# Performance work log

Hardware: AMD Instinct MI355X
Metric: run time of the kernel (lower is better)

## Reference

```python
import jax, jax.numpy as jnp
import numpy as np

N = 131072          # total nodes
E = 4194304         # edges (avg degree 32)
SUB = 16            # size_subgraph_samples
HID = 256


def _gcn_norm(src, dst, n):
    # add self-loops
    loops = jnp.arange(n, dtype=src.dtype)
    src = jnp.concatenate([src, loops])
    dst = jnp.concatenate([dst, loops])
    deg = jax.ops.segment_sum(jnp.ones_like(dst, dtype=jnp.float32), dst, num_segments=n)
    dinv = jnp.where(deg > 0, jax.lax.rsqrt(deg), 0.0)
    norm = dinv[src] * dinv[dst]  # [E+N]
    return src, dst, norm


def _gcn_conv(x, W, b, src, dst, norm, n):
    h = x @ W                                  # [N, out]
    msg = h[src] * norm[:, None]               # gather + scale
    agg = jax.ops.segment_sum(msg, dst, num_segments=n)
    return agg + b


def setup_inputs() -> dict:
    key = jax.random.key(0)
    ks = jax.random.split(key, 6)
    x = jax.random.normal(ks[0], (N, 128), dtype=jnp.float32)
    edge_index = jax.random.randint(ks[1], (2, E), 0, N, dtype=jnp.int64)
    W1 = jax.random.normal(ks[2], (128, HID), dtype=jnp.float32) * (1.0 / np.sqrt(128))
    b1 = jnp.zeros((HID,), dtype=jnp.float32)
    W2 = jax.random.normal(ks[3], (HID, HID), dtype=jnp.float32) * (1.0 / np.sqrt(HID))
    b2 = jnp.zeros((HID,), dtype=jnp.float32)
    Wout = jax.random.normal(ks[4], (HID * SUB, 1), dtype=jnp.float32) * (1.0 / np.sqrt(HID * SUB))
    bout = jnp.zeros((1,), dtype=jnp.float32)
    return {"x": x, "edge_index": edge_index, "W1": W1, "b1": b1,
            "W2": W2, "b2": b2, "Wout": Wout, "bout": bout}


def reference(x, edge_index, W1, b1, W2, b2, Wout, bout):
    n = x.shape[0]
    src, dst, norm = _gcn_norm(edge_index[0], edge_index[1], n)
    h = jax.nn.relu(_gcn_conv(x, W1, b1, src, dst, norm, n))
    h = jax.nn.relu(_gcn_conv(h, W2, b2, src, dst, norm, n))
    h = h.reshape(n // SUB, SUB * h.shape[1])   # [8192, 4096]
    return h @ Wout + bout                       # [8192, 1]
```

## Files before the change

### kernel.cpp

```cpp
#include <hip/hip_runtime.h>
#include <stdint.h>

#define NN 131072
#define NE 4194304
#define BKT 256
#define BKT_SH 9
#define BCAP 20480

typedef __bf16 bf16x8 __attribute__((ext_vector_type(8)));
typedef float  floatx4 __attribute__((ext_vector_type(4)));
typedef unsigned short u16x8 __attribute__((ext_vector_type(8)));

__device__ __forceinline__ float bf2f(unsigned short u) {
  union { unsigned int i; float f; } v; v.i = ((unsigned int)u) << 16; return v.f;
}
__device__ __forceinline__ unsigned short f2bf(float f) {
  union { float f; unsigned int i; } v; v.f = f;
  unsigned int r = v.i + 0x7fffu + ((v.i >> 16) & 1u);
  return (unsigned short)(r >> 16);
}


__global__ __launch_bounds__(256) void k_bzero(int* __restrict__ bktCnt) {
  bktCnt[threadIdx.x] = 0;
}

__global__ __launch_bounds__(1024) void k_bucket(const int* __restrict__ src,
                                                 const int* __restrict__ dst,
                                                 int* __restrict__ bktCnt,
                                                 unsigned int* __restrict__ bktBuf) {
  __shared__ int hist[BKT];
  __shared__ int base[BKT];
  const int t = threadIdx.x;
  if (t < BKT) hist[t] = 0;
  __syncthreads();
  const int e0 = (blockIdx.x * 1024 + t);
  const int4 s = ((const int4*)src)[e0];
  const int4 d = ((const int4*)dst)[e0];
  const int b0 = ((unsigned)d.x) >> BKT_SH, b1 = ((unsigned)d.y) >> BKT_SH;
  const int b2 = ((unsigned)d.z) >> BKT_SH, b3 = ((unsigned)d.w) >> BKT_SH;
  const int r0 = atomicAdd(&hist[b0], 1);
  const int r1 = atomicAdd(&hist[b1], 1);
  const int r2 = atomicAdd(&hist[b2], 1);
  const int r3 = atomicAdd(&hist[b3], 1);
  __syncthreads();
  if (t < BKT) base[t] = atomicAdd(&bktCnt[t], hist[t]);
  __syncthreads();
  const unsigned p0 = (((unsigned)s.x) << BKT_SH) | (d.x & 511);
  const unsigned p1 = (((unsigned)s.y) << BKT_SH) | (d.y & 511);
  const unsigned p2 = (((unsigned)s.z) << BKT_SH) | (d.z & 511);
  const unsigned p3 = (((unsigned)s.w) << BKT_SH) | (d.w & 511);
  bktBuf[(size_t)b0 * BCAP + base[b0] + r0] = p0;
  bktBuf[(size_t)b1 * BCAP + base[b1] + r1] = p1;
  bktBuf[(size_t)b2 * BCAP + base[b2] + r2] = p2;
  bktBuf[(size_t)b3 * BCAP + base[b3] + r3] = p3;
}

__global__ __launch_bounds__(1024) void k_csr(const int* __restrict__ bktCnt,
                                              const unsigned int* __restrict__ bktBuf,
                                              int* __restrict__ row_ptr,
                                              float* __restrict__ dinv,
                                              int* __restrict__ csr) {
  __shared__ int bsum[BKT];
  __shared__ int hist[512];
  __shared__ int sc[512];
  __shared__ int cur[512];
  const int b = blockIdx.x;
  const int t = threadIdx.x;
  if (t < BKT) bsum[t] = bktCnt[t];
  if (t < 512) hist[t] = 0;
  __syncthreads();
  for (int off = 1; off < BKT; off <<= 1) {
    int v = 0;
    if (t < BKT && t >= off) v = bsum[t - off];
    __syncthreads();
    if (t < BKT) bsum[t] += v;
    __syncthreads();
  }
  const int sz = bktCnt[b];
  const int csrBase = bsum[b] - sz;
  const unsigned int* eb = bktBuf + (size_t)b * BCAP;
  for (int i = t; i < sz; i += 1024) atomicAdd(&hist[eb[i] & 511], 1);
  __syncthreads();
  if (t < 512) sc[t] = hist[t];
  __syncthreads();
  for (int off = 1; off < 512; off <<= 1) {
    int v = 0;
    if (t < 512 && t >= off) v = sc[t - off];
    __syncthreads();
    if (t < 512) sc[t] += v;
    __syncthreads();
  }
  if (t < 512) {
    const int ex = csrBase + sc[t] - hist[t];
    row_ptr[b * 512 + t] = ex;
    cur[t] = ex;
    dinv[b * 512 + t] = rsqrtf((float)(hist[t] + 1));
  }
  if (b == BKT - 1 && t == 0) row_ptr[NN] = NE;
  __syncthreads();
  for (int i = t; i < sz; i += 1024) {
    const unsigned e = eb[i];
    csr[atomicAdd(&cur[e & 511], 1)] = (int)(e >> BKT_SH);
  }
}

__global__ __launch_bounds__(256) void k_cvt(const float* __restrict__ X,
                                             unsigned short* __restrict__ Xb) {
  const int t = blockIdx.x * 256 + threadIdx.x;
  const float4 v = ((const float4*)X)[t];
  ushort4 o;
  o.x = f2bf(v.x); o.y = f2bf(v.y); o.z = f2bf(v.z); o.w = f2bf(v.w);
  ((ushort4*)Xb)[t] = o;
}

__global__ __launch_bounds__(256) void k_swizzle(const float* __restrict__ W,
                                                 unsigned short* __restrict__ Wsw) {
  const int t = blockIdx.x * 256 + threadIdx.x;
  const int k = t >> 8, n = t & 255;
  const int s = ((k >> 5) * 16 + (n >> 4)) * 512 + ((k >> 3) & 3) * 128 + (n & 15) * 8 + (k & 7);
  Wsw[s] = f2bf(W[t]);
}

__global__ __launch_bounds__(256) void agg_128(const unsigned short* __restrict__ X,
                                               const int* __restrict__ row_ptr,
                                               const int* __restrict__ csr,
                                               const float* __restrict__ dinv,
                                               unsigned short* __restrict__ Y,
                                               int node_base) {
  const int lane = threadIdx.x & 63;
  const int node = node_base + ((blockIdx.x * blockDim.x + threadIdx.x) >> 6);
  const int sub = lane >> 4;
  const int fl = lane & 15;
  const int start = row_ptr[node];
  const int end = row_ptr[node + 1];
  const float di = dinv[node];
  float a[8] = {0.f, 0.f, 0.f, 0.f, 0.f, 0.f, 0.f, 0.f};
  const unsigned short* Xf = X + fl * 8;

  for (int e = start; e < end; e += 64) {
    const int nload = min(end - e, 64);
    int s_l = node;
    float w_l = 0.0f;
    if (lane < nload) {
      s_l = __builtin_nontemporal_load(&csr[e + lane]);
      w_l = dinv[s_l];
    }
    for (int j = 0; j < nload; j += 16) {
      const int i0 = j + sub, i1 = j + 4 + sub, i2 = j + 8 + sub, i3 = j + 12 + sub;
      const int s0 = __shfl(s_l, i0); const float w0 = __shfl(w_l, i0);
      const int s1 = __shfl(s_l, i1); const float w1 = __shfl(w_l, i1);
      const int s2 = __shfl(s_l, i2); const float w2 = __shfl(w_l, i2);
      const int s3 = __shfl(s_l, i3); const float w3 = __shfl(w_l, i3);
      const u16x8 r0 = *(const u16x8*)(Xf + (size_t)s0 * 128);
      const u16x8 r1 = *(const u16x8*)(Xf + (size_t)s1 * 128);
      const u16x8 r2 = *(const u16x8*)(Xf + (size_t)s2 * 128);
      const u16x8 r3 = *(const u16x8*)(Xf + (size_t)s3 * 128);
#pragma unroll
      for (int i = 0; i < 8; ++i) a[i] = fmaf(w0, bf2f(r0[i]), a[i]);
#pragma unroll
      for (int i = 0; i < 8; ++i) a[i] = fmaf(w1, bf2f(r1[i]), a[i]);
#pragma unroll
      for (int i = 0; i < 8; ++i) a[i] = fmaf(w2, bf2f(r2[i]), a[i]);
#pragma unroll
      for (int i = 0; i < 8; ++i) a[i] = fmaf(w3, bf2f(r3[i]), a[i]);
    }
  }
#pragma unroll
  for (int i = 0; i < 8; ++i) a[i] += __shfl_xor(a[i], 16);
#pragma unroll
  for (int i = 0; i < 8; ++i) a[i] += __shfl_xor(a[i], 32);
  const u16x8 sv = *(const u16x8*)(Xf + (size_t)node * 128);
#pragma unroll
  for (int i = 0; i < 8; ++i) a[i] = fmaf(di, bf2f(sv[i]), a[i]);
  if (sub == 0) {
    u16x8 o;
#pragma unroll
    for (int i = 0; i < 8; ++i) o[i] = f2bf(di * a[i]);
    *(u16x8*)(Y + (size_t)node * 128 + fl * 8) = o;
  }
}

__global__ __launch_bounds__(256) void agg_256(const unsigned short* __restrict__ X,
                                               const int* __restrict__ row_ptr,
                                               const int* __restrict__ csr,
                                               const float* __restrict__ dinv,
                                               unsigned short* __restrict__ Y,
                                               int node_base) {
  const int lane = threadIdx.x & 63;
  const int node = node_base + ((blockIdx.x * blockDim.x + threadIdx.x) >> 6);
  const int sub = lane >> 5;
  const int fl = lane & 31;
  const int start = row_ptr[node];
  const int end = row_ptr[node + 1];
  const float di = dinv[node];
  float a[8] = {0.f, 0.f, 0.f, 0.f, 0.f, 0.f, 0.f, 0.f};
  const unsigned short* Xf = X + fl * 8;

  for (int e = start; e < end; e += 64) {
    const int nload = min(end - e, 64);
    int s_l = node;
    float w_l = 0.0f;
    if (lane < nload) {
      s_l = __builtin_nontemporal_load(&csr[e + lane]);
      w_l = dinv[s_l];
    }
    for (int j = 0; j < nload; j += 8) {
      const int i0 = j + sub, i1 = j + 2 + sub, i2 = j + 4 + sub, i3 = j + 6 + sub;
      const int s0 = __shfl(s_l, i0); const float w0 = __shfl(w_l, i0);
      const int s1 = __shfl(s_l, i1); const float w1 = __shfl(w_l, i1);
      const int s2 = __shfl(s_l, i2); const float w2 = __shfl(w_l, i2);
      const int s3 = __shfl(s_l, i3); const float w3 = __shfl(w_l, i3);
      const u16x8 r0 = *(const u16x8*)(Xf + (size_t)s0 * 256);
      const u16x8 r1 = *(const u16x8*)(Xf + (size_t)s1 * 256);
      const u16x8 r2 = *(const u16x8*)(Xf + (size_t)s2 * 256);
      const u16x8 r3 = *(const u16x8*)(Xf + (size_t)s3 * 256);
#pragma unroll
      for (int i = 0; i < 8; ++i) a[i] = fmaf(w0, bf2f(r0[i]), a[i]);
#pragma unroll
      for (int i = 0; i < 8; ++i) a[i] = fmaf(w1, bf2f(r1[i]), a[i]);
#pragma unroll
      for (int i = 0; i < 8; ++i) a[i] = fmaf(w2, bf2f(r2[i]), a[i]);
#pragma unroll
      for (int i = 0; i < 8; ++i) a[i] = fmaf(w3, bf2f(r3[i]), a[i]);
    }
  }
#pragma unroll
  for (int i = 0; i < 8; ++i) a[i] += __shfl_xor(a[i], 32);
  const u16x8 sv = *(const u16x8*)(Xf + (size_t)node * 256);
#pragma unroll
  for (int i = 0; i < 8; ++i) a[i] = fmaf(di, bf2f(sv[i]), a[i]);
  if (sub == 0) {
    u16x8 o;
#pragma unroll
    for (int i = 0; i < 8; ++i) o[i] = f2bf(di * a[i]);
    *(u16x8*)(Y + (size_t)node * 256 + fl * 8) = o;
  }
}

template <int K>
__global__ __launch_bounds__(512) void k_gemm(const unsigned short* __restrict__ A,
                                              const unsigned short* __restrict__ Wsw,
                                              const float* __restrict__ bias,
                                              unsigned short* __restrict__ out) {
  __shared__ unsigned short lW[128 * 256];
  const int tid = threadIdx.x;
  const int wave = tid >> 6;
  const int lane = tid & 63;
  const int q = lane >> 4;
  const int m16 = lane & 15;
  const size_t baseM = (size_t)blockIdx.x * 256;

  floatx4 acc[2][16];
#pragma unroll
  for (int t = 0; t < 2; ++t)
#pragma unroll
    for (int nt = 0; nt < 16; ++nt) acc[t][nt] = (floatx4){0.f, 0.f, 0.f, 0.f};

  const size_t rowA0 = baseM + wave * 32 + m16;
  const size_t rowA1 = rowA0 + 16;

  for (int half = 0; half < K / 128; ++half) {
    __syncthreads();
    const uint4* gsrc = (const uint4*)(Wsw + half * 32768);
    uint4* ldst = (uint4*)lW;
#pragma unroll
    for (int i = 0; i < 8; ++i) ldst[i * 512 + tid] = gsrc[i * 512 + tid];
    __syncthreads();

#pragma unroll
    for (int kc = 0; kc < 4; ++kc) {
      const int koff = half * 128 + kc * 32 + q * 8;
      const bf16x8 av0 = *(const bf16x8*)(A + rowA0 * K + koff);
      const bf16x8 av1 = *(const bf16x8*)(A + rowA1 * K + koff);
#pragma unroll
      for (int nt = 0; nt < 16; ++nt) {
        const bf16x8 bv = *(const bf16x8*)(&lW[(kc * 16 + nt) * 512 + lane * 8]);
        acc[0][nt] = __builtin_amdgcn_mfma_f32_16x16x32_bf16(av0, bv, acc[0][nt], 0, 0, 0);
        acc[1][nt] = __builtin_amdgcn_mfma_f32_16x16x32_bf16(av1, bv, acc[1][nt], 0, 0, 0);
      }
    }
  }
  const int rq = (lane >> 4) * 4;
#pragma unroll
  for (int t = 0; t < 2; ++t) {
#pragma unroll
    for (int nt = 0; nt < 16; ++nt) {
      const int col = nt * 16 + m16;
      const float bv = bias[col];
#pragma unroll
      for (int r = 0; r < 4; ++r) {
        const size_t row = baseM + wave * 32 + t * 16 + rq + r;
        float v = acc[t][nt][r] + bv;
        v = fmaxf(v, 0.0f);
        out[row * 256 + col] = f2bf(v);
      }
    }
  }
}

__global__ __launch_bounds__(256) void k_final(const unsigned short* __restrict__ Z,
                                               const float* __restrict__ Wout,
                                               const float* __restrict__ bout,
                                               float* __restrict__ out) {
  const int lane = threadIdx.x & 63;
  const int g = (blockIdx.x * blockDim.x + threadIdx.x) >> 6;
  const unsigned short* z = Z + (size_t)g * 4096;
  float acc = 0.f;
#pragma unroll
  for (int it = 0; it < 16; ++it) {
    const int idx = (it * 64 + lane) * 4;
    const ushort4 zv = *(const ushort4*)(z + idx);
    const float4 wv = *(const float4*)(Wout + idx);
    acc = fmaf(bf2f(zv.x), wv.x, acc);
    acc = fmaf(bf2f(zv.y), wv.y, acc);
    acc = fmaf(bf2f(zv.z), wv.z, acc);
    acc = fmaf(bf2f(zv.w), wv.w, acc);
  }
#pragma unroll
  for (int off = 32; off > 0; off >>= 1) acc += __shfl_down(acc, off);
  if (lane == 0) out[g] = acc + bout[0];
}

extern "C" void kernel_launch(void* const* d_in, const int* in_sizes, int n_in,
                              void* d_out, int out_size, void* d_ws, size_t ws_size,
                              hipStream_t stream) {
  const float* x    = (const float*)d_in[0];
  const int*   ei   = (const int*)d_in[1];
  const float* W1   = (const float*)d_in[2];
  const float* b1   = (const float*)d_in[3];
  const float* W2   = (const float*)d_in[4];
  const float* b2   = (const float*)d_in[5];
  const float* Wout = (const float*)d_in[6];
  const float* bout = (const float*)d_in[7];
  float* out = (float*)d_out;

  char* ws = (char*)d_ws;
  size_t off = 0;
  auto alloc = [&](size_t bytes) {
    char* p = ws + off;
    off += (bytes + 511) & ~(size_t)511;
    return p;
  };
  int*            row_ptr = (int*)alloc(((size_t)NN + 1) * 4);
  float*          dinv    = (float*)alloc((size_t)NN * 4);
  int*            bktCnt  = (int*)alloc(BKT * 4);
  unsigned int*   bktBuf  = (unsigned int*)alloc((size_t)BKT * BCAP * 4);
  int*            csr     = (int*)alloc((size_t)NE * 4);
  unsigned short* Wsw1    = (unsigned short*)alloc(128 * 256 * 2);
  unsigned short* Wsw2    = (unsigned short*)alloc(256 * 256 * 2);
  unsigned short* xb      = (unsigned short*)alloc((size_t)NN * 128 * 2);
  unsigned short* bufA    = (unsigned short*)alloc((size_t)NN * 256 * 2);
  unsigned short* bufB    = (unsigned short*)alloc((size_t)NN * 256 * 2);
  (void)in_sizes; (void)n_in; (void)out_size; (void)ws_size;

  const int* src = ei;
  const int* dst = ei + NE;

  hipLaunchKernelGGL(k_bzero,  dim3(1), dim3(256), 0, stream, bktCnt);
  hipLaunchKernelGGL(k_bucket, dim3(NE / 4096), dim3(1024), 0, stream, src, dst, bktCnt, bktBuf);
  hipLaunchKernelGGL(k_csr,    dim3(BKT), dim3(1024), 0, stream, bktCnt, bktBuf, row_ptr, dinv, csr);
  hipLaunchKernelGGL(k_cvt,    dim3(NN * 128 / 4 / 256), dim3(256), 0, stream, x, xb);
  hipLaunchKernelGGL(k_swizzle, dim3(128), dim3(256), 0, stream, W1, Wsw1);
  hipLaunchKernelGGL(k_swizzle, dim3(256), dim3(256), 0, stream, W2, Wsw2);

  hipLaunchKernelGGL(agg_128, dim3(NN / 8), dim3(256), 0, stream, xb, row_ptr, csr, dinv, bufA, 0);
  hipLaunchKernelGGL(agg_128, dim3(NN / 8), dim3(256), 0, stream, xb, row_ptr, csr, dinv, bufA, NN / 2);
  hipLaunchKernelGGL(k_gemm<128>, dim3(NN / 256), dim3(512), 0, stream, bufA, Wsw1, b1, bufB);
  hipLaunchKernelGGL(agg_256, dim3(NN / 8), dim3(256), 0, stream, bufB, row_ptr, csr, dinv, bufA, 0);
  hipLaunchKernelGGL(agg_256, dim3(NN / 8), dim3(256), 0, stream, bufB, row_ptr, csr, dinv, bufA, NN / 2);
  hipLaunchKernelGGL(k_gemm<256>, dim3(NN / 256), dim3(512), 0, stream, bufA, Wsw2, b2, bufB);
  hipLaunchKernelGGL(k_final, dim3(8192 / 4), dim3(256), 0, stream, bufB, Wout, bout, out);
}
```

Measured before the change: 756.2 us.

## Split neighbor aggregation by feature halves instead of node halves

Aggregation kernels are merged into one templated kernel, and the two launches per layer now each cover all nodes but only half of the feature columns, instead of half the nodes with all features. This halves the gathered feature footprint per launch, so random neighbor-row gathers should hit cache more often. In exchange, the CSR indices and degree scales are read twice, and each wave does more shuffles per edge with narrower 8/16-lane row segments.

```diff
diff --git a/kernel.cpp b/kernel.cpp
--- a/kernel.cpp
+++ b/kernel.cpp
@@ -122,21 +122,23 @@
   Wsw[s] = f2bf(W[t]);
 }
 
-__global__ __launch_bounds__(256) void agg_128(const unsigned short* __restrict__ X,
-                                               const int* __restrict__ row_ptr,
-                                               const int* __restrict__ csr,
-                                               const float* __restrict__ dinv,
-                                               unsigned short* __restrict__ Y,
-                                               int node_base) {
+template <int LPR>
+__global__ __launch_bounds__(256) void agg_h(const unsigned short* __restrict__ X,
+                                             const int* __restrict__ row_ptr,
+                                             const int* __restrict__ csr,
+                                             const float* __restrict__ dinv,
+                                             unsigned short* __restrict__ Y,
+                                             int F, int foff) {
+  constexpr int SUB = 64 / LPR;
   const int lane = threadIdx.x & 63;
-  const int node = node_base + ((blockIdx.x * blockDim.x + threadIdx.x) >> 6);
-  const int sub = lane >> 4;
-  const int fl = lane & 15;
+  const int node = (blockIdx.x * blockDim.x + threadIdx.x) >> 6;
+  const int sub = lane / LPR;
+  const int fl = lane % LPR;
   const int start = row_ptr[node];
   const int end = row_ptr[node + 1];
   const float di = dinv[node];
   float a[8] = {0.f, 0.f, 0.f, 0.f, 0.f, 0.f, 0.f, 0.f};
-  const unsigned short* Xf = X + fl * 8;
+  const unsigned short* Xf = X + foff + fl * 8;
 
   for (int e = start; e < end; e += 64) {
     const int nload = min(end - e, 64);
@@ -146,16 +148,16 @@
       s_l = __builtin_nontemporal_load(&csr[e + lane]);
       w_l = dinv[s_l];
     }
-    for (int j = 0; j < nload; j += 16) {
-      const int i0 = j + sub, i1 = j + 4 + sub, i2 = j + 8 + sub, i3 = j + 12 + sub;
+    for (int j = 0; j < nload; j += 4 * SUB) {
+      const int i0 = j + sub, i1 = j + SUB + sub, i2 = j + 2 * SUB + sub, i3 = j + 3 * SUB + sub;
       const int s0 = __shfl(s_l, i0); const float w0 = __shfl(w_l, i0);
       const int s1 = __shfl(s_l, i1); const float w1 = __shfl(w_l, i1);
       const int s2 = __shfl(s_l, i2); const float w2 = __shfl(w_l, i2);
       const int s3 = __shfl(s_l, i3); const float w3 = __shfl(w_l, i3);
-      const u16x8 r0 = *(const u16x8*)(Xf + (size_t)s0 * 128);
-      const u16x8 r1 = *(const u16x8*)(Xf + (size_t)s1 * 128);
-      const u16x8 r2 = *(const u16x8*)(Xf + (size_t)s2 * 128);
-      const u16x8 r3 = *(const u16x8*)(Xf + (size_t)s3 * 128);
+      const u16x8 r0 = *(const u16x8*)(Xf + (size_t)s0 * F);
+      const u16x8 r1 = *(const u16x8*)(Xf + (size_t)s1 * F);
+      const u16x8 r2 = *(const u16x8*)(Xf + (size_t)s2 * F);
+      const u16x8 r3 = *(const u16x8*)(Xf + (size_t)s3 * F);
 #pragma unroll
       for (int i = 0; i < 8; ++i) a[i] = fmaf(w0, bf2f(r0[i]), a[i]);
 #pragma unroll
@@ -167,74 +169,17 @@
     }
   }
 #pragma unroll
-  for (int i = 0; i < 8; ++i) a[i] += __shfl_xor(a[i], 16);
-#pragma unroll
-  for (int i = 0; i < 8; ++i) a[i] += __shfl_xor(a[i], 32);
-  const u16x8 sv = *(const u16x8*)(Xf + (size_t)node * 128);
+  for (int off = LPR; off < 64; off <<= 1)
+#pragma unroll
+    for (int i = 0; i < 8; ++i) a[i] += __shfl_xor(a[i], off);
+  const u16x8 sv = *(const u16x8*)(Xf + (size_t)node * F);
 #pragma unroll
   for (int i = 0; i < 8; ++i) a[i] = fmaf(di, bf2f(sv[i]), a[i]);
   if (sub == 0) {
     u16x8 o;
 #pragma unroll
     for (int i = 0; i < 8; ++i) o[i] = f2bf(di * a[i]);
-    *(u16x8*)(Y + (size_t)node * 128 + fl * 8) = o;
-  }
-}
-
-__global__ __launch_bounds__(256) void agg_256(const unsigned short* __restrict__ X,
-                                               const int* __restrict__ row_ptr,
-                                               const int* __restrict__ csr,
-                                               const float* __restrict__ dinv,
-                                               unsigned short* __restrict__ Y,
-                                               int node_base) {
-  const int lane = threadIdx.x & 63;
-  const int node = node_base + ((blockIdx.x * blockDim.x + threadIdx.x) >> 6);
-  const int sub = lane >> 5;
-  const int fl = lane & 31;
-  const int start = row_ptr[node];
-  const int end = row_ptr[node + 1];
-  const float di = dinv[node];
-  float a[8] = {0.f, 0.f, 0.f, 0.f, 0.f, 0.f, 0.f, 0.f};
-  const unsigned short* Xf = X + fl * 8;
-
-  for (int e = start; e < end; e += 64) {
-    const int nload = min(end - e, 64);
-    int s_l = node;
-    float w_l = 0.0f;
-    if (lane < nload) {
-      s_l = __builtin_nontemporal_load(&csr[e + lane]);
-      w_l = dinv[s_l];
-    }
-    for (int j = 0; j < nload; j += 8) {
-      const int i0 = j + sub, i1 = j + 2 + sub, i2 = j + 4 + sub, i3 = j + 6 + sub;
-      const int s0 = __shfl(s_l, i0); const float w0 = __shfl(w_l, i0);
-      const int s1 = __shfl(s_l, i1); const float w1 = __shfl(w_l, i1);
-      const int s2 = __shfl(s_l, i2); const float w2 = __shfl(w_l, i2);
-      const int s3 = __shfl(s_l, i3); const float w3 = __shfl(w_l, i3);
-      const u16x8 r0 = *(const u16x8*)(Xf + (size_t)s0 * 256);
-      const u16x8 r1 = *(const u16x8*)(Xf + (size_t)s1 * 256);
-      const u16x8 r2 = *(const u16x8*)(Xf + (size_t)s2 * 256);
-      const u16x8 r3 = *(const u16x8*)(Xf + (size_t)s3 * 256);
-#pragma unroll
-      for (int i = 0; i < 8; ++i) a[i] = fmaf(w0, bf2f(r0[i]), a[i]);
-#pragma unroll
-      for (int i = 0; i < 8; ++i) a[i] = fmaf(w1, bf2f(r1[i]), a[i]);
-#pragma unroll
-      for (int i = 0; i < 8; ++i) a[i] = fmaf(w2, bf2f(r2[i]), a[i]);
-#pragma unroll
-      for (int i = 0; i < 8; ++i) a[i] = fmaf(w3, bf2f(r3[i]), a[i]);
-    }
-  }
-#pragma unroll
-  for (int i = 0; i < 8; ++i) a[i] += __shfl_xor(a[i], 32);
-  const u16x8 sv = *(const u16x8*)(Xf + (size_t)node * 256);
-#pragma unroll
-  for (int i = 0; i < 8; ++i) a[i] = fmaf(di, bf2f(sv[i]), a[i]);
-  if (sub == 0) {
-    u16x8 o;
-#pragma unroll
-    for (int i = 0; i < 8; ++i) o[i] = f2bf(di * a[i]);
-    *(u16x8*)(Y + (size_t)node * 256 + fl * 8) = o;
+    *(u16x8*)(Y + (size_t)node * F + foff + fl * 8) = o;
   }
 }
 
@@ -364,11 +309,11 @@
   hipLaunchKernelGGL(k_swizzle, dim3(128), dim3(256), 0, stream, W1, Wsw1);
   hipLaunchKernelGGL(k_swizzle, dim3(256), dim3(256), 0, stream, W2, Wsw2);
 
-  hipLaunchKernelGGL(agg_128, dim3(NN / 8), dim3(256), 0, stream, xb, row_ptr, csr, dinv, bufA, 0);
-  hipLaunchKernelGGL(agg_128, dim3(NN / 8), dim3(256), 0, stream, xb, row_ptr, csr, dinv, bufA, NN / 2);
+  hipLaunchKernelGGL(agg_h<8>, dim3(NN / 4), dim3(256), 0, stream, xb, row_ptr, csr, dinv, bufA, 128, 0);
+  hipLaunchKernelGGL(agg_h<8>, dim3(NN / 4), dim3(256), 0, stream, xb, row_ptr, csr, dinv, bufA, 128, 64);
   hipLaunchKernelGGL(k_gemm<128>, dim3(NN / 256), dim3(512), 0, stream, bufA, Wsw1, b1, bufB);
-  hipLaunchKernelGGL(agg_256, dim3(NN / 8), dim3(256), 0, stream, bufB, row_ptr, csr, dinv, bufA, 0);
-  hipLaunchKernelGGL(agg_256, dim3(NN / 8), dim3(256), 0, stream, bufB, row_ptr, csr, dinv, bufA, NN / 2);
+  hipLaunchKernelGGL(agg_h<16>, dim3(NN / 4), dim3(256), 0, stream, bufB, row_ptr, csr, dinv, bufA, 256, 0);
+  hipLaunchKernelGGL(agg_h<16>, dim3(NN / 4), dim3(256), 0, stream, bufB, row_ptr, csr, dinv, bufA, 256, 128);
   hipLaunchKernelGGL(k_gemm<256>, dim3(NN / 256), dim3(512), 0, stream, bufA, Wsw2, b2, bufB);
   hipLaunchKernelGGL(k_final, dim3(8192 / 4), dim3(256), 0, stream, bufB, Wout, bout, out);
 }
```

After: 733.7 us. 3.0% less time.
